# Kernel tuning notes

Measured on AMD Instinct MI355X. Metric: run time of the kernel, lower is better.

## Reference

```python
import jax, jax.numpy as jnp
import numpy as np

B = 512; S = 6; Q = 2            # meta-batch, n_way*k_shot, n_way*q_query
DIM = 64; IMG = 28; N_WAY = 2
HEADS = 4; HD = DIM // HEADS     # retrieval heads / head dim
EPS = 1e-5


def _pool_mat(inp, out):
    # exact torch AdaptiveAvgPool2d windowing as a matrix [out, inp]
    P = np.zeros((out, inp), np.float32)
    for i in range(out):
        s = (i * inp) // out
        e = -((-(i + 1) * inp) // out)
        P[i, s:e] = 1.0 / (e - s)
    return jnp.asarray(P)

P28 = _pool_mat(IMG, 8)  # 28 -> 8; subsequent 8 -> 8 pools are identity


def _gelu(x):
    return jax.nn.gelu(x, approximate=False)


def _conv(x, w, b):
    y = jax.lax.conv_general_dilated(x, w, (1, 1), ((1, 1), (1, 1)),
                                     dimension_numbers=('NCHW', 'OIHW', 'NCHW'))
    return y + b[None, :, None, None]


def _bn(x, p):
    # p rows: gamma, beta, running_mean, running_var (eval-mode BatchNorm2d)
    g, bt, m, v = p[0], p[1], p[2], p[3]
    sc = g / jnp.sqrt(v + EPS)
    return (x - m[None, :, None, None]) * sc[None, :, None, None] + bt[None, :, None, None]


def _img_in(x, c1w, c1b, bn1, c2w, c2b, bn2, c3w, c3b, bn3, c4w, c4b, bn4, lin_w):
    h = _bn(_conv(x, c1w, c1b), bn1)
    h = jnp.einsum('oi,ncij,pj->ncop', P28, h, P28)   # adaptive avg pool 28x28 -> 8x8
    h = _gelu(h)                                       # dropout is identity in eval
    h = _gelu(_bn(_conv(h, c2w, c2b), bn2))
    h = _gelu(_bn(_conv(h, c3w, c3b), bn3))
    h = _gelu(_bn(_conv(h, c4w, c4b), bn4))            # -> [N,1,8,8]
    h = h.reshape(h.shape[0], -1)                      # [N,64]
    return h @ lin_w.T                                 # Linear(64 -> DIM, no bias)


def _net(x, w1, w2):
    # x: [B,K,D]; w1,w2: [B,D,D] batched fast weights
    h = jnp.einsum('bed,bkd->bke', w1, x)
    ah = _gelu(h)
    y = jnp.einsum('bed,bkd->bke', w2, ah)
    return y, h


def _get_lor(x, w1, w2, r_q, r_k, r_v, r_o, ln_w, ln_b):
    b, k, _ = x.shape
    q, _ = _net(x, w1, w2)
    qh = jnp.einsum('nhd,bkd->bknh', r_q, q)
    sc = jnp.einsum('bknh,rnh->bknr', qh, r_k) / (HD ** 0.5)
    p = jax.nn.softmax(sc, axis=-1)
    lor = jnp.einsum('bknr,rnh->bknh', p, r_v).reshape(b, k, DIM)
    lor = jnp.einsum('de,bkd->bke', r_o, lor)
    z = lor + x
    mu = z.mean(-1, keepdims=True)
    var = ((z - mu) ** 2).mean(-1, keepdims=True)
    return (z - mu) / jnp.sqrt(var + EPS) * ln_w + ln_b


def _forward(query_w, sxs, qxs, inner_lr, c1w, c1b, bn1, c2w, c2b, bn2, c3w, c3b, bn3,
             c4w, c4b, bn4, lin_w, emb, w1, w2, tags, r_q, r_k, r_v, r_o, ln_w, ln_b,
             sys, qys):
    b = query_w.shape[0]
    s = sxs.shape[1]
    q = qxs.shape[1]
    feats = lambda im: _img_in(im.reshape(-1, 1, IMG, IMG), c1w, c1b, bn1, c2w, c2b,
                               bn2, c3w, c3b, bn3, c4w, c4b, bn4, lin_w)
    sx = feats(sxs).reshape(b, s, DIM)
    qx = feats(qxs).reshape(b, q, DIM)
    qe = tags[4]
    w1b = jnp.broadcast_to(w1, (b, DIM, DIM))
    w2b = jnp.broadcast_to(w2, (b, DIM, DIM))
    bound = sx + emb[sys]                                          # [B,S,D]
    # all 4 tag variants for all S shots in one vectorized get_lor call
    inp = (bound[:, :, None, :] + tags[:4][None, None]).reshape(b, s * 4, DIM)
    lors = _get_lor(inp, w1b, w2b, r_q, r_k, r_v, r_o, ln_w, ln_b).reshape(b, s, 4, DIM)
    l1s, r1s, l2s, r2s = lors[:, :, 0], lors[:, :, 1], lors[:, :, 2], lors[:, :, 3]
    qw1 = w1[None] + jnp.einsum('bsl,bsr->blr', l1s, r1s)
    qw2 = w2[None] + jnp.einsum('bsl,bsr->blr', l2s, r2s)
    preds, _ = _net(qx + qe, qw1, qw2)                             # [B,Q,D]
    logits = jnp.einsum('ld,bqd->bql', emb, preds).reshape(-1, N_WAY)
    labels = qys.reshape(-1)
    ls = jax.nn.log_softmax(logits)
    task_loss = -jnp.take_along_axis(ls, labels[:, None], axis=1).mean()
    n_correct = (jnp.argmax(logits, axis=1) == labels).sum()
    return task_loss, n_correct, b * q


def setup_inputs() -> dict:
    key = jax.random.key(0)
    ks = jax.random.split(key, 24)
    rn = lambda i, sh, sc=1.0: sc * jax.random.normal(ks[i], sh, jnp.float32)
    def bnp(i, c):
        k0, k1, k2 = jax.random.split(ks[i], 3)
        return jnp.stack([1.0 + 0.1 * jax.random.normal(k0, (c,)),
                          0.1 * jax.random.normal(k1, (c,)),
                          0.1 * jax.random.normal(k2, (c,)),
                          0.5 + jax.random.uniform(jax.random.fold_in(ks[i], 3), (c,))])
    return {
        'query_w': rn(0, (B, DIM)),
        'sxs': rn(1, (B, S, IMG * IMG)),
        'qxs': rn(2, (B, Q, IMG * IMG)),
        'inner_lr': jnp.float32(0.1),
        'c1w': rn(3, (32, 1, 3, 3), 0.3), 'c1b': rn(4, (32,), 0.1), 'bn1': bnp(5, 32),
        'c2w': rn(6, (32, 32, 3, 3), 0.06), 'c2b': rn(7, (32,), 0.1), 'bn2': bnp(8, 32),
        'c3w': rn(9, (32, 32, 3, 3), 0.06), 'c3b': rn(10, (32,), 0.1), 'bn3': bnp(11, 32),
        'c4w': rn(12, (1, 32, 3, 3), 0.06), 'c4b': rn(13, (1,), 0.1), 'bn4': bnp(14, 1),
        'lin_w': rn(15, (DIM, 64), 0.125),
        'emb': rn(16, (N_WAY, DIM), 0.125),
        'w1': rn(17, (DIM, DIM), 0.125),
        'w2': rn(18, (DIM, DIM), 0.125),
        'tags': rn(19, (8, DIM), 0.125),
        'r_q': rn(20, (HEADS, HD, DIM), 0.125),
        'r_k': rn(21, (16, HEADS, HD), 0.25),
        'r_v': rn(22, (16, HEADS, HD), 0.25),
        'r_o': rn(23, (DIM, DIM), 0.125),
        'ln_w': 0.001 * jnp.ones((DIM,), jnp.float32),
        'ln_b': jnp.zeros((DIM,), jnp.float32),
        'sys': jax.random.randint(jax.random.fold_in(key, 100), (B, S), 0, N_WAY),
        'qys': jax.random.randint(jax.random.fold_in(key, 101), (B, Q), 0, N_WAY),
    }


def reference(query_w, sxs, qxs, inner_lr, c1w, c1b, bn1, c2w, c2b, bn2, c3w, c3b, bn3,
              c4w, c4b, bn4, lin_w, emb, w1, w2, tags, r_q, r_k, r_v, r_o, ln_w, ln_b,
              sys, qys):
    task_loss, n_correct, n_q = _forward(query_w, sxs, qxs, inner_lr, c1w, c1b, bn1,
                                         c2w, c2b, bn2, c3w, c3b, bn3, c4w, c4b, bn4,
                                         lin_w, emb, w1, w2, tags, r_q, r_k, r_v, r_o,
                                         ln_w, ln_b, sys, qys)
    return (task_loss, task_loss, jnp.float32(0.0), n_correct, n_q)
```

## Files before the change

kernel.cpp:

```cpp
#include <hip/hip_runtime.h>
#include <math.h>

constexpr float EPSF = 1e-5f;

constexpr int WS_W1B  = 0;
constexpr int WS_B1   = 1024;
constexpr int WS_W2B  = 1056;
constexpr int WS_W3B  = 5664;
constexpr int WS_W4B  = 10272;
constexpr int WS_B4   = 10416;
constexpr int WS_B2   = 10420;
constexpr int WS_B3   = 10452;
constexpr int WS_HW1  = 10484;
constexpr int WS_HM   = 12788;
constexpr int WS_HW2  = 15092;
constexpr int WS_HROT = 17396;
constexpr int WS_RKB  = 19700;
constexpr int WS_RVT  = 20212;
constexpr int WS_PART = 20724;
constexpr int WS_CNT  = 21748;

constexpr int ACT_CS  = 816;
constexpr int ACT_SZ  = 4 * ACT_CS;

using short8 = __attribute__((ext_vector_type(8))) short;
using f32x4  = __attribute__((ext_vector_type(4))) float;

__device__ __forceinline__ float gelu_f(float x) {
    float z  = fabsf(x) * 0.70710678118654752440f;
    float t  = __builtin_amdgcn_rcpf(__builtin_fmaf(0.3275911f, z, 1.0f));
    float p  = t * __builtin_fmaf(t,
                 __builtin_fmaf(t,
                   __builtin_fmaf(t,
                     __builtin_fmaf(t, 1.061405429f, -1.453152027f),
                     1.421413741f),
                   -0.284496736f),
                 0.254829592f);
    float e  = __expf(-z * z);
    float er = __builtin_fmaf(-p, e, 1.0f);
    float s  = copysignf(er, x);
    return 0.5f * x * (1.0f + s);
}
__device__ __forceinline__ unsigned short f2bf(float f) {
    unsigned u = __float_as_uint(f);
    return (unsigned short)((u + 0x7FFFu + ((u >> 16) & 1u)) >> 16);
}
__device__ __forceinline__ float bflo(unsigned u) { return __uint_as_float(u << 16); }
__device__ __forceinline__ float bfhi(unsigned u) { return __uint_as_float(u & 0xffff0000u); }

__global__ void __launch_bounds__(256) precompute_kernel(
    const float* __restrict__ c1w, const float* __restrict__ c1b, const float* __restrict__ bn1,
    const float* __restrict__ c2w, const float* __restrict__ c2b, const float* __restrict__ bn2,
    const float* __restrict__ c3w, const float* __restrict__ c3b, const float* __restrict__ bn3,
    const float* __restrict__ c4w, const float* __restrict__ c4b, const float* __restrict__ bn4,
    const float* __restrict__ w1, const float* __restrict__ w2,
    const float* __restrict__ rq, const float* __restrict__ ro,
    const float* __restrict__ rk, const float* __restrict__ rv,
    float* __restrict__ ws)
{
    const int gid = blockIdx.x * 256 + threadIdx.x;
    const int gsz = gridDim.x * 256;

    if (gid == 0) *((unsigned*)(ws + WS_CNT)) = 0u;

    unsigned short* w1b = (unsigned short*)(ws + WS_W1B);
    for (int v = gid; v < 2048; v += gsz) {
        int c8 = v & 7, colx = (v >> 3) & 15, qd = (v >> 7) & 3, hh = (v >> 9) & 1, kt = v >> 10;
        int tap = kt * 32 + qd * 8 + c8;
        int oc = hh * 16 + colx;
        unsigned short o = 0;
        if (tap < 36) {
            int tt = tap / 6, s = tap - tt * 6;
            float sum = 0.f;
            for (int di = 0; di < 3; ++di) {
                int a = tt - di; if (a < 0 || a > 3) continue;
                for (int dj = 0; dj < 3; ++dj) {
                    int bb = s - dj; if (bb < 0 || bb > 3) continue;
                    sum += c1w[oc * 9 + di * 3 + dj];
                }
            }
            float sc1 = bn1[oc] * rsqrtf(bn1[96 + oc] + EPSF);
            o = f2bf(sum * sc1 * (1.0f / 16.0f));
        }
        w1b[v] = o;
    }
    for (int c = gid; c < 32; c += gsz) {
        float sc1 = bn1[c] * rsqrtf(bn1[96 + c] + EPSF);
        ws[WS_B1 + c] = (c1b[c] - bn1[64 + c]) * sc1 + bn1[32 + c];
        float sc2 = bn2[c] * rsqrtf(bn2[96 + c] + EPSF);
        ws[WS_B2 + c] = (c2b[c] - bn2[64 + c]) * sc2 + bn2[32 + c];
        float sc3 = bn3[c] * rsqrtf(bn3[96 + c] + EPSF);
        ws[WS_B3 + c] = (c3b[c] - bn3[64 + c]) * sc3 + bn3[32 + c];
    }
    unsigned short* w2b = (unsigned short*)(ws + WS_W2B);
    unsigned short* w3b = (unsigned short*)(ws + WS_W3B);
    for (int v = gid; v < 9216; v += gsz) {
        int c8 = v & 7, colx = (v >> 3) & 15, qd = (v >> 7) & 3, hh = (v >> 9) & 1, tap = v >> 10;
        int oc = hh * 16 + colx;
        int ic = qd * 8 + c8;
        float sc2 = bn2[oc] * rsqrtf(bn2[96 + oc] + EPSF);
        float sc3 = bn3[oc] * rsqrtf(bn3[96 + oc] + EPSF);
        w2b[v] = f2bf(c2w[oc * 288 + ic * 9 + tap] * sc2);
        w3b[v] = f2bf(c3w[oc * 288 + ic * 9 + tap] * sc3);
    }
    {
        unsigned short* w4b = (unsigned short*)(ws + WS_W4B);
        float sc4 = bn4[0] * rsqrtf(bn4[3] + EPSF);
        for (int v = gid; v < 288; v += gsz) {
            int tap = v >> 5, ic = v & 31;
            w4b[v] = f2bf(c4w[ic * 9 + tap] * sc4);
        }
        if (gid == 0) ws[WS_B4] = (c4b[0] - bn4[2]) * sc4 + bn4[1];
    }
    unsigned short* hw1 = (unsigned short*)(ws + WS_HW1);
    unsigned short* hm  = (unsigned short*)(ws + WS_HM);
    unsigned short* hw2 = (unsigned short*)(ws + WS_HW2);
    unsigned short* hro = (unsigned short*)(ws + WS_HROT);
    for (int v = gid; v < 4608; v += gsz) {
        int e = v / 72, d = v - e * 72;
        unsigned short a = 0, b = 0, c = 0, r = 0;
        if (d < 64) {
            a = f2bf(w1[e * 64 + d]);
            b = f2bf(w2[e * 64 + d]);
            float m = 0.f;
            for (int q = 0; q < 64; ++q) m += rq[e * 64 + q] * w2[q * 64 + d];
            c = f2bf(m);
            r = f2bf(ro[d * 64 + e]);
        }
        hw1[v] = a; hw2[v] = b; hm[v] = c; hro[v] = r;
    }
    unsigned short* rkb = (unsigned short*)(ws + WS_RKB);
    unsigned short* rvt = (unsigned short*)(ws + WS_RVT);
    for (int v = gid; v < 1024; v += gsz) {
        int nn = v >> 8, x = (v >> 4) & 15, y = v & 15;
        rkb[v] = f2bf(rk[x * 64 + nn * 16 + y] * 0.25f);
        rvt[v] = f2bf(rv[y * 64 + nn * 16 + x]);
    }
}

struct FeatsSmem {
    unsigned short sAct[8][ACT_SZ];
    float          sh4[8][64];
};
struct HeadSmem {
    unsigned short sP[2048];
};
union FusedSmem {
    FeatsSmem f;
    HeadSmem  h;
};

__device__ __forceinline__ void conv32g(const unsigned short* __restrict__ A,
                                        const unsigned short* __restrict__ Wg,
                                        int col, int quad, f32x4 (&acc)[4][2])
{
    int ab[4];
    #pragma unroll
    for (int mt = 0; mt < 4; ++mt) {
        int px = mt * 16 + col;
        ab[mt] = quad * ACT_CS + ((px >> 3) * 10 + (px & 7)) * 8;
        acc[mt][0] = (f32x4){0,0,0,0};
        acc[mt][1] = (f32x4){0,0,0,0};
    }
    #pragma unroll
    for (int dr = 0; dr < 3; ++dr)
        #pragma unroll
        for (int dc = 0; dc < 3; ++dc) {
            int tap = dr * 3 + dc;
            short8 b0 = *(const short8*)(Wg + (((tap * 2 + 0) * 4 + quad) * 16 + col) * 8);
            short8 b1 = *(const short8*)(Wg + (((tap * 2 + 1) * 4 + quad) * 16 + col) * 8);
            #pragma unroll
            for (int mt = 0; mt < 4; ++mt) {
                short8 a = *(const short8*)(A + ab[mt] + (dr * 10 + dc) * 8);
                acc[mt][0] = __builtin_amdgcn_mfma_f32_16x16x32_bf16(a, b0, acc[mt][0], 0, 0, 0);
                acc[mt][1] = __builtin_amdgcn_mfma_f32_16x16x32_bf16(a, b1, acc[mt][1], 0, 0, 0);
            }
        }
}

__device__ __forceinline__ void conv_store4(unsigned short* __restrict__ A,
                                            const f32x4 (&acc)[4][2],
                                            float bi0, float bi1, int col, int quad)
{
    #pragma unroll
    for (int mt = 0; mt < 4; ++mt)
        #pragma unroll
        for (int reg = 0; reg < 4; ++reg) {
            int px = mt * 16 + quad * 4 + reg;
            int P = ((px >> 3) + 1) * 10 + (px & 7) + 1;
            A[(col >> 3) * ACT_CS + P * 8 + (col & 7)]       = f2bf(gelu_f(acc[mt][0][reg] + bi0));
            A[(2 + (col >> 3)) * ACT_CS + P * 8 + (col & 7)] = f2bf(gelu_f(acc[mt][1][reg] + bi1));
        }
}

__device__ __forceinline__ f32x4 head_gemm8(const unsigned short* __restrict__ Ab,
                                            const unsigned short* __restrict__ Bw,
                                            int col, int quad, int wvid)
{
    int mt = wvid & 1, nt = wvid >> 1;
    f32x4 acc = {0, 0, 0, 0};
    #pragma unroll
    for (int kt = 0; kt < 2; ++kt) {
        short8 a = *(const short8*)(Ab + (mt * 16 + col) * 72 + kt * 32 + quad * 8);
        short8 b = *(const short8*)(Bw + (nt * 16 + col) * 72 + kt * 32 + quad * 8);
        acc = __builtin_amdgcn_mfma_f32_16x16x32_bf16(a, b, acc, 0, 0, 0);
    }
    return acc;
}

__global__ void __launch_bounds__(512, 4) fused_kernel(
    const float* __restrict__ sxs, const float* __restrict__ qxs,
    const float* __restrict__ lin_w,
    const float* __restrict__ emb, const float* __restrict__ tags,
    const float* __restrict__ lnw, const float* __restrict__ lnb,
    const int* __restrict__ sys, const int* __restrict__ qys,
    float* __restrict__ ws, float* __restrict__ out)
{
    __shared__ __align__(16) FusedSmem sm;
    __shared__ __align__(16) unsigned short bufA[2304], bufB[2304];
    __shared__ __align__(16) float sXf[1536];
    __shared__ __align__(16) float s_xq[128], s_ah[128], s_yp[128];
    __shared__ float s_t1[12], s_t2[12], s_lg[4], s_red[16];
    __shared__ int s_last;

    const int t    = threadIdx.x;
    const int b    = blockIdx.x;
    const int wv   = t >> 6;
    const int lane = t & 63;
    const int col  = lane & 15;
    const int quad = lane >> 4;

    float embv = 0.f, tg0 = 0.f, tg1 = 0.f, tg2 = 0.f, tg3 = 0.f, tgq = 0.f;
    if (wv < 6) {
        int cls = sys[b * 6 + wv];
        embv = emb[cls * 64 + lane];
        tg0 = tags[0 * 64 + lane];
        tg1 = tags[1 * 64 + lane];
        tg2 = tags[2 * 64 + lane];
        tg3 = tags[3 * 64 + lane];
    } else {
        tgq = tags[256 + lane];
    }
    if (t < 72) {
        uint4 z = {0, 0, 0, 0};
        ((uint4*)(bufA + 1728))[t] = z;
        ((uint4*)(bufB + 1728))[t] = z;
    }

    {
        unsigned short* A = sm.f.sAct[wv];
        float bi1a = ws[WS_B1 + col], bi1b = ws[WS_B1 + 16 + col];
        float bi2a = ws[WS_B2 + col], bi2b = ws[WS_B2 + 16 + col];
        float bi3a = ws[WS_B3 + col], bi3b = ws[WS_B3 + 16 + col];
        float b4   = ws[WS_B4];

        {
            const float* img = (wv < 6) ? (sxs + ((size_t)b * 6 + wv) * 784)
                                        : (qxs + ((size_t)b * 2 + (wv - 6)) * 784);
            const float4* sv = (const float4*)img;
            #pragma unroll
            for (int j = 0; j < 4; ++j) {
                int idx = j * 64 + lane;
                if (idx < 196) {
                    float4 v = sv[idx];
                    ushort4 o = { f2bf(v.x), f2bf(v.y), f2bf(v.z), f2bf(v.w) };
                    *(ushort4*)(A + idx * 4) = o;
                }
            }
        }

        f32x4 acc[4][2];
        {
            const unsigned short* w1g = (const unsigned short*)(ws + WS_W1B);
            short8 b00 = *(const short8*)(w1g + ((0 * 4 + quad) * 16 + col) * 8);
            short8 b01 = *(const short8*)(w1g + ((1 * 4 + quad) * 16 + col) * 8);
            short8 b10 = *(const short8*)(w1g + ((2 * 4 + quad) * 16 + col) * 8);
            short8 b11 = *(const short8*)(w1g + ((3 * 4 + quad) * 16 + col) * 8);
            int ttj[8], ssj[8];
            #pragma unroll
            for (int j = 0; j < 8; ++j) {
                int k = quad * 8 + j;
                ttj[j] = k / 6; ssj[j] = k - ttj[j] * 6;
            }
            #pragma unroll
            for (int mt = 0; mt < 4; ++mt) {
                acc[mt][0] = (f32x4){0,0,0,0};
                acc[mt][1] = (f32x4){0,0,0,0};
                int px = mt * 16 + col;
                int sr = (((px >> 3) * 7) >> 1) - 1;
                int sc = (((px & 7) * 7) >> 1) - 1;
                short8 a0;
                #pragma unroll
                for (int j = 0; j < 8; ++j) {
                    int rr = sr + ttj[j], cc = sc + ssj[j];
                    bool ok = ((unsigned)rr < 28u) && ((unsigned)cc < 28u);
                    int off = ok ? (rr * 28 + cc) : 0;
                    unsigned short hv = A[off];
                    a0[j] = ok ? (short)hv : (short)0;
                }
                acc[mt][0] = __builtin_amdgcn_mfma_f32_16x16x32_bf16(a0, b00, acc[mt][0], 0, 0, 0);
                acc[mt][1] = __builtin_amdgcn_mfma_f32_16x16x32_bf16(a0, b01, acc[mt][1], 0, 0, 0);
                short8 a1 = {0,0,0,0,0,0,0,0};
                if (quad == 0) {
                    #pragma unroll
                    for (int j = 0; j < 4; ++j) {
                        int rr = sr + 5, cc = sc + 2 + j;
                        bool ok = ((unsigned)rr < 28u) && ((unsigned)cc < 28u);
                        int off = ok ? (rr * 28 + cc) : 0;
                        unsigned short hv = A[off];
                        a1[j] = ok ? (short)hv : (short)0;
                    }
                }
                acc[mt][0] = __builtin_amdgcn_mfma_f32_16x16x32_bf16(a1, b10, acc[mt][0], 0, 0, 0);
                acc[mt][1] = __builtin_amdgcn_mfma_f32_16x16x32_bf16(a1, b11, acc[mt][1], 0, 0, 0);
            }
        }
        {
            uint4 z4 = {0, 0, 0, 0};
            #pragma unroll
            for (int it = 0; it < 3; ++it) {
                int h = lane + it * 64;
                if (h < 144) {
                    int pi = h >> 2, ch = h & 3;
                    int P;
                    if (pi < 10)      P = pi;
                    else if (pi < 20) P = 90 + (pi - 10);
                    else { int k = pi - 20; int r = 1 + (k >> 1); P = r * 10 + (k & 1) * 9; }
                    ((uint4*)A)[ch * (ACT_CS / 8) + P] = z4;
                }
            }
        }
        conv_store4(A, acc, bi1a, bi1b, col, quad);

        conv32g(A, (const unsigned short*)(ws + WS_W2B), col, quad, acc);
        conv_store4(A, acc, bi2a, bi2b, col, quad);
        conv32g(A, (const unsigned short*)(ws + WS_W3B), col, quad, acc);
        conv_store4(A, acc, bi3a, bi3b, col, quad);

        {
            f32x4 acc4[4];
            int ab[4];
            #pragma unroll
            for (int mt = 0; mt < 4; ++mt) {
                int px = mt * 16 + col;
                ab[mt] = quad * ACT_CS + ((px >> 3) * 10 + (px & 7)) * 8;
                acc4[mt] = (f32x4){0,0,0,0};
            }
            const unsigned short* w4g = (const unsigned short*)(ws + WS_W4B);
            #pragma unroll
            for (int dr = 0; dr < 3; ++dr)
                #pragma unroll
                for (int dc = 0; dc < 3; ++dc) {
                    int tap = dr * 3 + dc;
                    short8 bb = *(const short8*)(w4g + tap * 32 + quad * 8);
                    #pragma unroll
                    for (int mt = 0; mt < 4; ++mt) {
                        short8 a = *(const short8*)(A + ab[mt] + (dr * 10 + dc) * 8);
                        acc4[mt] = __builtin_amdgcn_mfma_f32_16x16x32_bf16(a, bb, acc4[mt], 0, 0, 0);
                    }
                }
            if (col < 4) {
                f32x4 v = acc4[0];
                if (col == 1) v = acc4[1];
                else if (col == 2) v = acc4[2];
                else if (col == 3) v = acc4[3];
                #pragma unroll
                for (int reg = 0; reg < 4; ++reg)
                    sm.f.sh4[wv][col * 16 + quad * 4 + reg] = gelu_f(v[reg] + b4);
            }
        }
        {
            const float4* lw = (const float4*)(lin_w + (size_t)lane * 64);
            const float4* hp = (const float4*)sm.f.sh4[wv];
            float acc2 = 0.f;
            #pragma unroll
            for (int j = 0; j < 16; ++j) {
                float4 w = lw[j], h = hp[j];
                acc2 += w.x * h.x + w.y * h.y + w.z * h.z + w.w * h.w;
            }
            if (wv < 6) {
                float base = acc2 + embv;
                float v0 = base + tg0, v1 = base + tg1, v2 = base + tg2, v3 = base + tg3;
                sXf[(wv * 4 + 0) * 64 + lane] = v0;
                sXf[(wv * 4 + 1) * 64 + lane] = v1;
                sXf[(wv * 4 + 2) * 64 + lane] = v2;
                sXf[(wv * 4 + 3) * 64 + lane] = v3;
                bufA[(wv * 4 + 0) * 72 + lane] = f2bf(v0);
                bufA[(wv * 4 + 1) * 72 + lane] = f2bf(v1);
                bufA[(wv * 4 + 2) * 72 + lane] = f2bf(v2);
                bufA[(wv * 4 + 3) * 72 + lane] = f2bf(v3);
            } else {
                s_xq[(wv - 6) * 64 + lane] = acc2 + tgq;
            }
        }
    }
    __syncthreads();

    const unsigned short* gW1 = (const unsigned short*)(ws + WS_HW1);
    const unsigned short* gM  = (const unsigned short*)(ws + WS_HM);
    const unsigned short* gW2 = (const unsigned short*)(ws + WS_HW2);
    const unsigned short* gRO = (const unsigned short*)(ws + WS_HROT);

    {
        f32x4 r = head_gemm8(bufA, gW1, col, quad, wv);
        int mt = wv & 1, nt = wv >> 1;
        #pragma unroll
        for (int reg = 0; reg < 4; ++reg) {
            int row = mt * 16 + quad * 4 + reg;
            if (row < 24) bufB[row * 72 + nt * 16 + col] = f2bf(gelu_f(r[reg]));
        }
    }
    __syncthreads();
    {
        f32x4 r = head_gemm8(bufB, gM, col, quad, wv);
        int mt = wv & 1, nt = wv >> 1;
        #pragma unroll
        for (int reg = 0; reg < 4; ++reg) {
            int row = mt * 16 + quad * 4 + reg;
            if (row < 24) bufA[row * 72 + nt * 16 + col] = f2bf(r[reg]);
        }
    }
    __syncthreads();

    if (wv < 4) {
        const int nh = wv;
        const unsigned short* rkB = (const unsigned short*)(ws + WS_RKB) + nh * 256;
        const unsigned short* rvT = (const unsigned short*)(ws + WS_RVT) + nh * 256;
        unsigned short* sP = sm.h.sP;
        const short8 zz = {0,0,0,0,0,0,0,0};
        const bool lo = (quad < 2);
        {
            int r8 = lane >> 3, c2 = lane & 7;
            *(unsigned int*)(sP + (24 + r8) * 64 + nh * 16 + c2 * 2) = 0u;
        }
        short8 bK = lo ? *(const short8*)(rkB + col * 16 + quad * 8) : zz;
        short8 a0 = lo ? *(const short8*)(bufA + col * 72 + nh * 16 + quad * 8) : zz;
        short8 a1 = lo ? *(const short8*)(bufA + (16 + col) * 72 + nh * 16 + quad * 8) : zz;
        f32x4 s0 = __builtin_amdgcn_mfma_f32_16x16x32_bf16(a0, bK, (f32x4){0,0,0,0}, 0, 0, 0);
        f32x4 s1 = __builtin_amdgcn_mfma_f32_16x16x32_bf16(a1, bK, (f32x4){0,0,0,0}, 0, 0, 0);
        #pragma unroll
        for (int reg = 0; reg < 4; ++reg) {
            float v = s0[reg];
            float m = v;
            m = fmaxf(m, __shfl_xor(m, 1)); m = fmaxf(m, __shfl_xor(m, 2));
            m = fmaxf(m, __shfl_xor(m, 4)); m = fmaxf(m, __shfl_xor(m, 8));
            float p = __expf(v - m);
            float su = p;
            su += __shfl_xor(su, 1); su += __shfl_xor(su, 2);
            su += __shfl_xor(su, 4); su += __shfl_xor(su, 8);
            sP[(quad * 4 + reg) * 64 + nh * 16 + col] = f2bf(p / su);
            v = s1[reg];
            m = v;
            m = fmaxf(m, __shfl_xor(m, 1)); m = fmaxf(m, __shfl_xor(m, 2));
            m = fmaxf(m, __shfl_xor(m, 4)); m = fmaxf(m, __shfl_xor(m, 8));
            p = __expf(v - m);
            su = p;
            su += __shfl_xor(su, 1); su += __shfl_xor(su, 2);
            su += __shfl_xor(su, 4); su += __shfl_xor(su, 8);
            if (quad < 2) sP[(16 + quad * 4 + reg) * 64 + nh * 16 + col] = f2bf(p / su);
        }
        short8 bV  = lo ? *(const short8*)(rvT + col * 16 + quad * 8) : zz;
        short8 pa0 = lo ? *(const short8*)(sP + col * 64 + nh * 16 + quad * 8) : zz;
        short8 pa1 = lo ? *(const short8*)(sP + (16 + col) * 64 + nh * 16 + quad * 8) : zz;
        f32x4 o0 = __builtin_amdgcn_mfma_f32_16x16x32_bf16(pa0, bV, (f32x4){0,0,0,0}, 0, 0, 0);
        f32x4 o1 = __builtin_amdgcn_mfma_f32_16x16x32_bf16(pa1, bV, (f32x4){0,0,0,0}, 0, 0, 0);
        #pragma unroll
        for (int reg = 0; reg < 4; ++reg) {
            bufA[(quad * 4 + reg) * 72 + nh * 16 + col] = f2bf(o0[reg]);
            int tok = 16 + quad * 4 + reg;
            if (tok < 24) bufA[tok * 72 + nh * 16 + col] = f2bf(o1[reg]);
        }
    }
    __syncthreads();

    {
        f32x4 r = head_gemm8(bufA, gRO, col, quad, wv);
        int mt = wv & 1, nt = wv >> 1;
        #pragma unroll
        for (int reg = 0; reg < 4; ++reg) {
            int row = mt * 16 + quad * 4 + reg;
            if (row < 24) {
                int idx = row * 64 + nt * 16 + col;
                sXf[idx] = sXf[idx] + r[reg];
            }
        }
    }
    __syncthreads();

    if (t < 192) {
        int k = t >> 3, j = t & 7;
        const float4* zp = (const float4*)(sXf + k * 64 + j * 8);
        float4 v0 = zp[0], v1 = zp[1];
        float sx_ = v0.x + v0.y + v0.z + v0.w + v1.x + v1.y + v1.z + v1.w;
        sx_ += __shfl_xor(sx_, 1); sx_ += __shfl_xor(sx_, 2); sx_ += __shfl_xor(sx_, 4);
        float mu = sx_ * (1.0f / 64.0f);
        float d0 = v0.x - mu, d1 = v0.y - mu, d2 = v0.z - mu, d3 = v0.w - mu;
        float d4 = v1.x - mu, d5 = v1.y - mu, d6 = v1.z - mu, d7 = v1.w - mu;
        float vv = d0*d0 + d1*d1 + d2*d2 + d3*d3 + d4*d4 + d5*d5 + d6*d6 + d7*d7;
        vv += __shfl_xor(vv, 1); vv += __shfl_xor(vv, 2); vv += __shfl_xor(vv, 4);
        float rs = 1.0f / sqrtf(vv * (1.0f / 64.0f) + EPSF);
        const float4* lwv = (const float4*)(lnw + j * 8);
        const float4* lbv = (const float4*)(lnb + j * 8);
        float4 w0 = lwv[0], w1_ = lwv[1], b0 = lbv[0], b1_ = lbv[1];
        ushort4 o0 = { f2bf(d0 * rs * w0.x + b0.x), f2bf(d1 * rs * w0.y + b0.y),
                       f2bf(d2 * rs * w0.z + b0.z), f2bf(d3 * rs * w0.w + b0.w) };
        ushort4 o1 = { f2bf(d4 * rs * w1_.x + b1_.x), f2bf(d5 * rs * w1_.y + b1_.y),
                       f2bf(d6 * rs * w1_.z + b1_.z), f2bf(d7 * rs * w1_.w + b1_.w) };
        *(ushort4*)(bufB + k * 72 + j * 8)     = o0;
        *(ushort4*)(bufB + k * 72 + j * 8 + 4) = o1;
    }
    __syncthreads();

    if (t < 96) {
        int idx = t >> 3, j = t & 7;
        int q = idx / 6, s = idx - q * 6;
        uint4 u = ((const uint4*)(bufB + (s * 4 + 1) * 72))[j];
        const float* x = s_xq + q * 64 + j * 8;
        float d = bflo(u.x)*x[0] + bfhi(u.x)*x[1] + bflo(u.y)*x[2] + bfhi(u.y)*x[3]
                + bflo(u.z)*x[4] + bfhi(u.z)*x[5] + bflo(u.w)*x[6] + bfhi(u.w)*x[7];
        d += __shfl_xor(d, 1); d += __shfl_xor(d, 2); d += __shfl_xor(d, 4);
        if (j == 0) s_t1[idx] = d;
    }
    __syncthreads();
    if (t < 128) {
        int q = t >> 6, e = t & 63;
        const uint4* wp = (const uint4*)(gW1 + e * 72);
        const float* xp = s_xq + q * 64;
        float acc = 0.f;
        #pragma unroll
        for (int j = 0; j < 8; ++j) {
            uint4 u = wp[j];
            const float* x = xp + j * 8;
            acc += bflo(u.x)*x[0] + bfhi(u.x)*x[1] + bflo(u.y)*x[2] + bfhi(u.y)*x[3]
                 + bflo(u.z)*x[4] + bfhi(u.z)*x[5] + bflo(u.w)*x[6] + bfhi(u.w)*x[7];
        }
        #pragma unroll
        for (int s = 0; s < 6; ++s)
            acc += bflo((unsigned)bufB[(s * 4 + 0) * 72 + e]) * s_t1[q * 6 + s];
        s_ah[t] = gelu_f(acc);
    }
    __syncthreads();
    if (t < 96) {
        int idx = t >> 3, j = t & 7;
        int q = idx / 6, s = idx - q * 6;
        uint4 u = ((const uint4*)(bufB + (s * 4 + 3) * 72))[j];
        const float* x = s_ah + q * 64 + j * 8;
        float d = bflo(u.x)*x[0] + bfhi(u.x)*x[1] + bflo(u.y)*x[2] + bfhi(u.y)*x[3]
                + bflo(u.z)*x[4] + bfhi(u.z)*x[5] + bflo(u.w)*x[6] + bfhi(u.w)*x[7];
        d += __shfl_xor(d, 1); d += __shfl_xor(d, 2); d += __shfl_xor(d, 4);
        if (j == 0) s_t2[idx] = d;
    }
    __syncthreads();
    if (t < 128) {
        int q = t >> 6, e = t & 63;
        const uint4* wp = (const uint4*)(gW2 + e * 72);
        const float* xp = s_ah + q * 64;
        float acc = 0.f;
        #pragma unroll
        for (int j = 0; j < 8; ++j) {
            uint4 u = wp[j];
            const float* x = xp + j * 8;
            acc += bflo(u.x)*x[0] + bfhi(u.x)*x[1] + bflo(u.y)*x[2] + bfhi(u.y)*x[3]
                 + bflo(u.z)*x[4] + bfhi(u.z)*x[5] + bflo(u.w)*x[6] + bfhi(u.w)*x[7];
        }
        #pragma unroll
        for (int s = 0; s < 6; ++s)
            acc += bflo((unsigned)bufB[(s * 4 + 2) * 72 + e]) * s_t2[q * 6 + s];
        s_yp[t] = acc;
    }
    __syncthreads();

    float* part = ws + WS_PART;
    if (t < 32) {
        int q = t >> 4, ll = (t >> 3) & 1, j = t & 7;
        const float* ep = emb + ll * 64 + j * 8;
        const float* yp = s_yp + q * 64 + j * 8;
        float d = ep[0]*yp[0] + ep[1]*yp[1] + ep[2]*yp[2] + ep[3]*yp[3]
                + ep[4]*yp[4] + ep[5]*yp[5] + ep[6]*yp[6] + ep[7]*yp[7];
        d += __shfl_xor(d, 1); d += __shfl_xor(d, 2); d += __shfl_xor(d, 4);
        if (j == 0) s_lg[q * 2 + ll] = d;
    }
    if (t == 0) {
        float lsum = 0.f, corr = 0.f;
        #pragma unroll
        for (int q = 0; q < 2; ++q) {
            float l0 = s_lg[q * 2], l1 = s_lg[q * 2 + 1];
            int lab = qys[b * 2 + q];
            float m = fmaxf(l0, l1);
            float lse = m + logf(expf(l0 - m) + expf(l1 - m));
            lsum += -((lab ? l1 : l0) - lse);
            int pred = (l1 > l0) ? 1 : 0;
            corr += (pred == lab) ? 1.0f : 0.0f;
        }
        part[b] = lsum;
        part[512 + b] = corr;
        __threadfence();
        unsigned old = atomicAdd((unsigned*)(ws + WS_CNT), 1u);
        s_last = (old == 511) ? 1 : 0;
    }
    __syncthreads();

    if (s_last) {
        __threadfence();
        float l = part[t];
        float c = part[512 + t];
        #pragma unroll
        for (int off = 1; off < 64; off <<= 1) {
            l += __shfl_xor(l, off);
            c += __shfl_xor(c, off);
        }
        if (lane == 0) { s_red[wv * 2] = l; s_red[wv * 2 + 1] = c; }
        __syncthreads();
        if (t == 0) {
            float L = 0.f, C = 0.f;
            #pragma unroll
            for (int w = 0; w < 8; ++w) { L += s_red[w * 2]; C += s_red[w * 2 + 1]; }
            float loss = L * (1.0f / 1024.0f);
            out[0] = loss;
            out[1] = loss;
            out[2] = 0.0f;
            out[3] = C;
            out[4] = 1024.0f;
        }
    }
}

extern "C" void kernel_launch(void* const* d_in, const int* in_sizes, int n_in,
                              void* d_out, int out_size, void* d_ws, size_t ws_size,
                              hipStream_t stream)
{
    (void)in_sizes; (void)n_in; (void)out_size; (void)ws_size;
    const float* sxs  = (const float*)d_in[1];
    const float* qxs  = (const float*)d_in[2];
    const float* c1w  = (const float*)d_in[4];
    const float* c1b  = (const float*)d_in[5];
    const float* bn1  = (const float*)d_in[6];
    const float* c2w  = (const float*)d_in[7];
    const float* c2b  = (const float*)d_in[8];
    const float* bn2  = (const float*)d_in[9];
    const float* c3w  = (const float*)d_in[10];
    const float* c3b  = (const float*)d_in[11];
    const float* bn3  = (const float*)d_in[12];
    const float* c4w  = (const float*)d_in[13];
    const float* c4b  = (const float*)d_in[14];
    const float* bn4  = (const float*)d_in[15];
    const float* lin_w= (const float*)d_in[16];
    const float* emb  = (const float*)d_in[17];
    const float* w1   = (const float*)d_in[18];
    const float* w2   = (const float*)d_in[19];
    const float* tags = (const float*)d_in[20];
    const float* rq   = (const float*)d_in[21];
    const float* rk   = (const float*)d_in[22];
    const float* rv   = (const float*)d_in[23];
    const float* ro   = (const float*)d_in[24];
    const float* lnw  = (const float*)d_in[25];
    const float* lnb  = (const float*)d_in[26];
    const int*   sys  = (const int*)d_in[27];
    const int*   qys  = (const int*)d_in[28];

    float* ws  = (float*)d_ws;
    float* out = (float*)d_out;

    precompute_kernel<<<64, 256, 0, stream>>>(c1w, c1b, bn1, c2w, c2b, bn2,
                                              c3w, c3b, bn3, c4w, c4b, bn4,
                                              w1, w2, rq, ro, rk, rv, ws);
    fused_kernel<<<512, 512, 0, stream>>>(sxs, qxs, lin_w, emb, tags, lnw, lnb,
                                          sys, qys, ws, out);
}
```

Baseline: 171.3 us.

## Process two meta-batch episodes per 1024-thread block with duplicated shared buffers

```diff
diff --git a/kernel.cpp b/kernel.cpp
--- a/kernel.cpp
+++ b/kernel.cpp
@@ -20,7 +20,7 @@
 constexpr int WS_PART = 20724;
 constexpr int WS_CNT  = 21748;
 
-constexpr int ACT_CS  = 816;
+constexpr int ACT_CS  = 808;
 constexpr int ACT_SZ  = 4 * ACT_CS;
 
 using short8 = __attribute__((ext_vector_type(8))) short;
@@ -139,11 +139,17 @@
 }
 
 struct FeatsSmem {
-    unsigned short sAct[8][ACT_SZ];
-    float          sh4[8][64];
+    unsigned short sAct[16][ACT_SZ];
+    float          sh4[16][64];
 };
 struct HeadSmem {
-    unsigned short sP[2048];
+    unsigned short bufB[2][2304];
+    unsigned short sP[2][2048];
+    float s_ah[2][128];
+    float s_yp[2][128];
+    float s_t1[2][12];
+    float s_t2[2][12];
+    float s_lg[2][4];
 };
 union FusedSmem {
     FeatsSmem f;
@@ -195,9 +201,9 @@
 
 __device__ __forceinline__ f32x4 head_gemm8(const unsigned short* __restrict__ Ab,
                                             const unsigned short* __restrict__ Bw,
-                                            int col, int quad, int wvid)
+                                            int col, int quad, int wvh)
 {
-    int mt = wvid & 1, nt = wvid >> 1;
+    int mt = wvh & 1, nt = wvh >> 1;
     f32x4 acc = {0, 0, 0, 0};
     #pragma unroll
     for (int kt = 0; kt < 2; ++kt) {
@@ -208,7 +214,7 @@
     return acc;
 }
 
-__global__ void __launch_bounds__(512, 4) fused_kernel(
+__global__ void __launch_bounds__(1024, 4) fused_kernel(
     const float* __restrict__ sxs, const float* __restrict__ qxs,
     const float* __restrict__ lin_w,
     const float* __restrict__ emb, const float* __restrict__ tags,
@@ -217,22 +223,27 @@
     float* __restrict__ ws, float* __restrict__ out)
 {
     __shared__ __align__(16) FusedSmem sm;
-    __shared__ __align__(16) unsigned short bufA[2304], bufB[2304];
-    __shared__ __align__(16) float sXf[1536];
-    __shared__ __align__(16) float s_xq[128], s_ah[128], s_yp[128];
-    __shared__ float s_t1[12], s_t2[12], s_lg[4], s_red[16];
-    __shared__ int s_last;
+    __shared__ __align__(16) unsigned short bufA[2][2304];
+    __shared__ __align__(16) float sXf[2][1536];
+    __shared__ __align__(16) float s_xq[2][128];
+    __shared__ float s_red[16];
+    __shared__ int s_lastv;
 
     const int t    = threadIdx.x;
-    const int b    = blockIdx.x;
+    const int tt   = t & 511;
+    const int eh   = t >> 9;
     const int wv   = t >> 6;
+    const int wvh  = wv & 7;
     const int lane = t & 63;
     const int col  = lane & 15;
     const int quad = lane >> 4;
+    const int be   = blockIdx.x * 2 + eh;
+
+    if (t == 0) s_lastv = 0;
 
     float embv = 0.f, tg0 = 0.f, tg1 = 0.f, tg2 = 0.f, tg3 = 0.f, tgq = 0.f;
-    if (wv < 6) {
-        int cls = sys[b * 6 + wv];
+    if (wvh < 6) {
+        int cls = sys[be * 6 + wvh];
         embv = emb[cls * 64 + lane];
         tg0 = tags[0 * 64 + lane];
         tg1 = tags[1 * 64 + lane];
@@ -241,10 +252,10 @@
     } else {
         tgq = tags[256 + lane];
     }
-    if (t < 72) {
+    if (t < 144) {
         uint4 z = {0, 0, 0, 0};
-        ((uint4*)(bufA + 1728))[t] = z;
-        ((uint4*)(bufB + 1728))[t] = z;
+        int e2 = t / 72, r = t - e2 * 72;
+        ((uint4*)(bufA[e2] + 1728))[r] = z;
     }
 
     {
@@ -255,8 +266,8 @@
         float b4   = ws[WS_B4];
 
         {
-            const float* img = (wv < 6) ? (sxs + ((size_t)b * 6 + wv) * 784)
-                                        : (qxs + ((size_t)b * 2 + (wv - 6)) * 784);
+            const float* img = (wvh < 6) ? (sxs + ((size_t)be * 6 + wvh) * 784)
+                                         : (qxs + ((size_t)be * 2 + (wvh - 6)) * 784);
             const float4* sv = (const float4*)img;
             #pragma unroll
             for (int j = 0; j < 4; ++j) {
@@ -378,19 +389,19 @@
                 float4 w = lw[j], h = hp[j];
                 acc2 += w.x * h.x + w.y * h.y + w.z * h.z + w.w * h.w;
             }
-            if (wv < 6) {
+            if (wvh < 6) {
                 float base = acc2 + embv;
                 float v0 = base + tg0, v1 = base + tg1, v2 = base + tg2, v3 = base + tg3;
-                sXf[(wv * 4 + 0) * 64 + lane] = v0;
-                sXf[(wv * 4 + 1) * 64 + lane] = v1;
-                sXf[(wv * 4 + 2) * 64 + lane] = v2;
-                sXf[(wv * 4 + 3) * 64 + lane] = v3;
-                bufA[(wv * 4 + 0) * 72 + lane] = f2bf(v0);
-                bufA[(wv * 4 + 1) * 72 + lane] = f2bf(v1);
-                bufA[(wv * 4 + 2) * 72 + lane] = f2bf(v2);
-                bufA[(wv * 4 + 3) * 72 + lane] = f2bf(v3);
+                sXf[eh][(wvh * 4 + 0) * 64 + lane] = v0;
+                sXf[eh][(wvh * 4 + 1) * 64 + lane] = v1;
+                sXf[eh][(wvh * 4 + 2) * 64 + lane] = v2;
+                sXf[eh][(wvh * 4 + 3) * 64 + lane] = v3;
+                bufA[eh][(wvh * 4 + 0) * 72 + lane] = f2bf(v0);
+                bufA[eh][(wvh * 4 + 1) * 72 + lane] = f2bf(v1);
+                bufA[eh][(wvh * 4 + 2) * 72 + lane] = f2bf(v2);
+                bufA[eh][(wvh * 4 + 3) * 72 + lane] = f2bf(v3);
             } else {
-                s_xq[(wv - 6) * 64 + lane] = acc2 + tgq;
+                s_xq[eh][(wvh - 6) * 64 + lane] = acc2 + tgq;
             }
         }
     }
@@ -401,32 +412,38 @@
     const unsigned short* gW2 = (const unsigned short*)(ws + WS_HW2);
     const unsigned short* gRO = (const unsigned short*)(ws + WS_HROT);
 
+    if (t < 144) {
+        uint4 z = {0, 0, 0, 0};
+        int e2 = t / 72, r = t - e2 * 72;
+        ((uint4*)(sm.h.bufB[e2] + 1728))[r] = z;
+    }
     {
-        f32x4 r = head_gemm8(bufA, gW1, col, quad, wv);
-        int mt = wv & 1, nt = wv >> 1;
+        f32x4 r = head_gemm8(bufA[eh], gW1, col, quad, wvh);
+        int mt = wvh & 1, nt = wvh >> 1;
         #pragma unroll
         for (int reg = 0; reg < 4; ++reg) {
             int row = mt * 16 + quad * 4 + reg;
-            if (row < 24) bufB[row * 72 + nt * 16 + col] = f2bf(gelu_f(r[reg]));
+            if (row < 24) sm.h.bufB[eh][row * 72 + nt * 16 + col] = f2bf(gelu_f(r[reg]));
         }
     }
     __syncthreads();
     {
-        f32x4 r = head_gemm8(bufB, gM, col, quad, wv);
-        int mt = wv & 1, nt = wv >> 1;
+        f32x4 r = head_gemm8(sm.h.bufB[eh], gM, col, quad, wvh);
+        int mt = wvh & 1, nt = wvh >> 1;
         #pragma unroll
         for (int reg = 0; reg < 4; ++reg) {
             int row = mt * 16 + quad * 4 + reg;
-            if (row < 24) bufA[row * 72 + nt * 16 + col] = f2bf(r[reg]);
-        }
-    }
-    __syncthreads();
-
-    if (wv < 4) {
-        const int nh = wv;
+            if (row < 24) bufA[eh][row * 72 + nt * 16 + col] = f2bf(r[reg]);
+        }
+    }
+    __syncthreads();
+
+    if (wvh < 4) {
+        const int nh = wvh;
         const unsigned short* rkB = (const unsigned short*)(ws + WS_RKB) + nh * 256;
         const unsigned short* rvT = (const unsigned short*)(ws + WS_RVT) + nh * 256;
-        unsigned short* sP = sm.h.sP;
+        unsigned short* bA = bufA[eh];
+        unsigned short* sP = sm.h.sP[eh];
         const short8 zz = {0,0,0,0,0,0,0,0};
         const bool lo = (quad < 2);
         {
@@ -434,8 +451,8 @@
             *(unsigned int*)(sP + (24 + r8) * 64 + nh * 16 + c2 * 2) = 0u;
         }
         short8 bK = lo ? *(const short8*)(rkB + col * 16 + quad * 8) : zz;
-        short8 a0 = lo ? *(const short8*)(bufA + col * 72 + nh * 16 + quad * 8) : zz;
-        short8 a1 = lo ? *(const short8*)(bufA + (16 + col) * 72 + nh * 16 + quad * 8) : zz;
+        short8 a0 = lo ? *(const short8*)(bA + col * 72 + nh * 16 + quad * 8) : zz;
+        short8 a1 = lo ? *(const short8*)(bA + (16 + col) * 72 + nh * 16 + quad * 8) : zz;
         f32x4 s0 = __builtin_amdgcn_mfma_f32_16x16x32_bf16(a0, bK, (f32x4){0,0,0,0}, 0, 0, 0);
         f32x4 s1 = __builtin_amdgcn_mfma_f32_16x16x32_bf16(a1, bK, (f32x4){0,0,0,0}, 0, 0, 0);
         #pragma unroll
@@ -466,30 +483,30 @@
         f32x4 o1 = __builtin_amdgcn_mfma_f32_16x16x32_bf16(pa1, bV, (f32x4){0,0,0,0}, 0, 0, 0);
         #pragma unroll
         for (int reg = 0; reg < 4; ++reg) {
-            bufA[(quad * 4 + reg) * 72 + nh * 16 + col] = f2bf(o0[reg]);
+            bA[(quad * 4 + reg) * 72 + nh * 16 + col] = f2bf(o0[reg]);
             int tok = 16 + quad * 4 + reg;
-            if (tok < 24) bufA[tok * 72 + nh * 16 + col] = f2bf(o1[reg]);
+            if (tok < 24) bA[tok * 72 + nh * 16 + col] = f2bf(o1[reg]);
         }
     }
     __syncthreads();
 
     {
-        f32x4 r = head_gemm8(bufA, gRO, col, quad, wv);
-        int mt = wv & 1, nt = wv >> 1;
+        f32x4 r = head_gemm8(bufA[eh], gRO, col, quad, wvh);
+        int mt = wvh & 1, nt = wvh >> 1;
         #pragma unroll
         for (int reg = 0; reg < 4; ++reg) {
             int row = mt * 16 + quad * 4 + reg;
             if (row < 24) {
                 int idx = row * 64 + nt * 16 + col;
-                sXf[idx] = sXf[idx] + r[reg];
-            }
-        }
-    }
-    __syncthreads();
-
-    if (t < 192) {
-        int k = t >> 3, j = t & 7;
-        const float4* zp = (const float4*)(sXf + k * 64 + j * 8);
+                sXf[eh][idx] = sXf[eh][idx] + r[reg];
+            }
+        }
+    }
+    __syncthreads();
+
+    if (tt < 192) {
+        int k = tt >> 3, j = tt & 7;
+        const float4* zp = (const float4*)(sXf[eh] + k * 64 + j * 8);
         float4 v0 = zp[0], v1 = zp[1];
         float sx_ = v0.x + v0.y + v0.z + v0.w + v1.x + v1.y + v1.z + v1.w;
         sx_ += __shfl_xor(sx_, 1); sx_ += __shfl_xor(sx_, 2); sx_ += __shfl_xor(sx_, 4);
@@ -506,26 +523,26 @@
                        f2bf(d2 * rs * w0.z + b0.z), f2bf(d3 * rs * w0.w + b0.w) };
         ushort4 o1 = { f2bf(d4 * rs * w1_.x + b1_.x), f2bf(d5 * rs * w1_.y + b1_.y),
                        f2bf(d6 * rs * w1_.z + b1_.z), f2bf(d7 * rs * w1_.w + b1_.w) };
-        *(ushort4*)(bufB + k * 72 + j * 8)     = o0;
-        *(ushort4*)(bufB + k * 72 + j * 8 + 4) = o1;
-    }
-    __syncthreads();
-
-    if (t < 96) {
-        int idx = t >> 3, j = t & 7;
+        *(ushort4*)(sm.h.bufB[eh] + k * 72 + j * 8)     = o0;
+        *(ushort4*)(sm.h.bufB[eh] + k * 72 + j * 8 + 4) = o1;
+    }
+    __syncthreads();
+
+    if (tt < 96) {
+        int idx = tt >> 3, j = tt & 7;
         int q = idx / 6, s = idx - q * 6;
-        uint4 u = ((const uint4*)(bufB + (s * 4 + 1) * 72))[j];
-        const float* x = s_xq + q * 64 + j * 8;
+        uint4 u = ((const uint4*)(sm.h.bufB[eh] + (s * 4 + 1) * 72))[j];
+        const float* x = s_xq[eh] + q * 64 + j * 8;
         float d = bflo(u.x)*x[0] + bfhi(u.x)*x[1] + bflo(u.y)*x[2] + bfhi(u.y)*x[3]
                 + bflo(u.z)*x[4] + bfhi(u.z)*x[5] + bflo(u.w)*x[6] + bfhi(u.w)*x[7];
         d += __shfl_xor(d, 1); d += __shfl_xor(d, 2); d += __shfl_xor(d, 4);
-        if (j == 0) s_t1[idx] = d;
-    }
-    __syncthreads();
-    if (t < 128) {
-        int q = t >> 6, e = t & 63;
-        const uint4* wp = (const uint4*)(gW1 + e * 72);
-        const float* xp = s_xq + q * 64;
+        if (j == 0) sm.h.s_t1[eh][idx] = d;
+    }
+    __syncthreads();
+    if (tt < 128) {
+        int q = tt >> 6, d = tt & 63;
+        const uint4* wp = (const uint4*)(gW1 + d * 72);
+        const float* xp = s_xq[eh] + q * 64;
         float acc = 0.f;
         #pragma unroll
         for (int j = 0; j < 8; ++j) {
@@ -536,25 +553,25 @@
         }
         #pragma unroll
         for (int s = 0; s < 6; ++s)
-            acc += bflo((unsigned)bufB[(s * 4 + 0) * 72 + e]) * s_t1[q * 6 + s];
-        s_ah[t] = gelu_f(acc);
-    }
-    __syncthreads();
-    if (t < 96) {
-        int idx = t >> 3, j = t & 7;
+            acc += bflo((unsigned)sm.h.bufB[eh][(s * 4 + 0) * 72 + d]) * sm.h.s_t1[eh][q * 6 + s];
+        sm.h.s_ah[eh][tt] = gelu_f(acc);
+    }
+    __syncthreads();
+    if (tt < 96) {
+        int idx = tt >> 3, j = tt & 7;
         int q = idx / 6, s = idx - q * 6;
-        uint4 u = ((const uint4*)(bufB + (s * 4 + 3) * 72))[j];
-        const float* x = s_ah + q * 64 + j * 8;
+        uint4 u = ((const uint4*)(sm.h.bufB[eh] + (s * 4 + 3) * 72))[j];
+        const float* x = sm.h.s_ah[eh] + q * 64 + j * 8;
         float d = bflo(u.x)*x[0] + bfhi(u.x)*x[1] + bflo(u.y)*x[2] + bfhi(u.y)*x[3]
                 + bflo(u.z)*x[4] + bfhi(u.z)*x[5] + bflo(u.w)*x[6] + bfhi(u.w)*x[7];
         d += __shfl_xor(d, 1); d += __shfl_xor(d, 2); d += __shfl_xor(d, 4);
-        if (j == 0) s_t2[idx] = d;
-    }
-    __syncthreads();
-    if (t < 128) {
-        int q = t >> 6, e = t & 63;
-        const uint4* wp = (const uint4*)(gW2 + e * 72);
-        const float* xp = s_ah + q * 64;
+        if (j == 0) sm.h.s_t2[eh][idx] = d;
+    }
+    __syncthreads();
+    if (tt < 128) {
+        int q = tt >> 6, d = tt & 63;
+        const uint4* wp = (const uint4*)(gW2 + d * 72);
+        const float* xp = sm.h.s_ah[eh] + q * 64;
         float acc = 0.f;
         #pragma unroll
         for (int j = 0; j < 8; ++j) {
@@ -565,51 +582,53 @@
         }
         #pragma unroll
         for (int s = 0; s < 6; ++s)
-            acc += bflo((unsigned)bufB[(s * 4 + 2) * 72 + e]) * s_t2[q * 6 + s];
-        s_yp[t] = acc;
+            acc += bflo((unsigned)sm.h.bufB[eh][(s * 4 + 2) * 72 + d]) * sm.h.s_t2[eh][q * 6 + s];
+        sm.h.s_yp[eh][tt] = acc;
     }
     __syncthreads();
 
     float* part = ws + WS_PART;
-    if (t < 32) {
-        int q = t >> 4, ll = (t >> 3) & 1, j = t & 7;
+    if (tt < 32) {
+        int q = tt >> 4, ll = (tt >> 3) & 1, j = tt & 7;
         const float* ep = emb + ll * 64 + j * 8;
-        const float* yp = s_yp + q * 64 + j * 8;
+        const float* yp = sm.h.s_yp[eh] + q * 64 + j * 8;
         float d = ep[0]*yp[0] + ep[1]*yp[1] + ep[2]*yp[2] + ep[3]*yp[3]
                 + ep[4]*yp[4] + ep[5]*yp[5] + ep[6]*yp[6] + ep[7]*yp[7];
         d += __shfl_xor(d, 1); d += __shfl_xor(d, 2); d += __shfl_xor(d, 4);
-        if (j == 0) s_lg[q * 2 + ll] = d;
-    }
-    if (t == 0) {
+        if (j == 0) sm.h.s_lg[eh][q * 2 + ll] = d;
+    }
+    if (tt == 0) {
         float lsum = 0.f, corr = 0.f;
         #pragma unroll
         for (int q = 0; q < 2; ++q) {
-            float l0 = s_lg[q * 2], l1 = s_lg[q * 2 + 1];
-            int lab = qys[b * 2 + q];
+            float l0 = sm.h.s_lg[eh][q * 2], l1 = sm.h.s_lg[eh][q * 2 + 1];
+            int lab = qys[be * 2 + q];
             float m = fmaxf(l0, l1);
             float lse = m + logf(expf(l0 - m) + expf(l1 - m));
             lsum += -((lab ? l1 : l0) - lse);
             int pred = (l1 > l0) ? 1 : 0;
             corr += (pred == lab) ? 1.0f : 0.0f;
         }
-        part[b] = lsum;
-        part[512 + b] = corr;
+        part[be] = lsum;
+        part[512 + be] = corr;
         __threadfence();
         unsigned old = atomicAdd((unsigned*)(ws + WS_CNT), 1u);
-        s_last = (old == 511) ? 1 : 0;
-    }
-    __syncthreads();
-
-    if (s_last) {
+        if (old == 511) s_lastv = 1;
+    }
+    __syncthreads();
+
+    if (s_lastv) {
         __threadfence();
-        float l = part[t];
-        float c = part[512 + t];
-        #pragma unroll
-        for (int off = 1; off < 64; off <<= 1) {
-            l += __shfl_xor(l, off);
-            c += __shfl_xor(c, off);
-        }
-        if (lane == 0) { s_red[wv * 2] = l; s_red[wv * 2 + 1] = c; }
+        if (t < 512) {
+            float l = part[t];
+            float c = part[512 + t];
+            #pragma unroll
+            for (int off = 1; off < 64; off <<= 1) {
+                l += __shfl_xor(l, off);
+                c += __shfl_xor(c, off);
+            }
+            if (lane == 0) { s_red[wv * 2] = l; s_red[wv * 2 + 1] = c; }
+        }
         __syncthreads();
         if (t == 0) {
             float L = 0.f, C = 0.f;
@@ -664,6 +683,6 @@
     precompute_kernel<<<64, 256, 0, stream>>>(c1w, c1b, bn1, c2w, c2b, bn2,
                                               c3w, c3b, bn3, c4w, c4b, bn4,
                                               w1, w2, rq, ro, rk, rv, ws);
-    fused_kernel<<<512, 512, 0, stream>>>(sxs, qxs, lin_w, emb, tags, lnw, lnb,
-                                          sys, qys, ws, out);
-}
+    fused_kernel<<<256, 1024, 0, stream>>>(sxs, qxs, lin_w, emb, tags, lnw, lnb,
+                                           sys, qys, ws, out);
+}
```

After: 173.1 us. Within noise of the previous version (+1.1%).
